# Kernel tuning notes

Measured on AMD Instinct MI355X. Metric: run time of the kernel, lower is better.

Reference implementation:

```python
import jax, jax.numpy as jnp
import numpy as np

B, S, E, H = 2, 2048, 1024, 16
D = E // H  # head_dim = 64


def setup_inputs() -> dict:
    key = jax.random.key(0)
    ks = jax.random.split(key, 14)
    inp = {
        "query": jax.random.normal(ks[0], (B, S, E), jnp.float32),
        "key": jax.random.normal(ks[1], (B, S, E), jnp.float32),
        "value": jax.random.normal(ks[2], (B, S, E), jnp.float32),
        "adj": jax.random.normal(ks[3], (S, S), jnp.float32),
        "mask": jax.random.randint(ks[4], (B, 1, S, S), 0, 2, jnp.int32),
    }
    sc = 1.0 / np.sqrt(E)
    inp["Wq"] = jax.random.normal(ks[5], (E, E), jnp.float32) * sc
    inp["bq"] = jax.random.normal(ks[6], (E,), jnp.float32) * sc
    inp["Wk"] = jax.random.normal(ks[7], (E, E), jnp.float32) * sc
    inp["bk"] = jax.random.normal(ks[8], (E,), jnp.float32) * sc
    inp["Wv"] = jax.random.normal(ks[9], (E, E), jnp.float32) * sc
    inp["bv"] = jax.random.normal(ks[10], (E,), jnp.float32) * sc
    inp["Wo"] = jax.random.normal(ks[11], (E, E), jnp.float32) * sc
    inp["bo"] = jax.random.normal(ks[12], (E,), jnp.float32) * sc
    return inp


def reference(query, key, value, adj, mask, Wq, bq, Wk, bk, Wv, bv, Wo, bo):
    b, s, _ = query.shape
    # projections, split into heads: [B,S,E] -> [B,H,S,D]
    def heads(x, W, bias):
        y = jnp.einsum("bse,ef->bsf", x, W.T) + bias
        return y.reshape(b, s, H, D).transpose(0, 2, 1, 3)

    Q = heads(query, Wq, bq)
    K = heads(key, Wk, bk)
    V = heads(value, Wv, bv)

    # scores: [B,H,S,S], scaled by sqrt(head_dim), plus adjacency bias
    scores = jnp.einsum("bhqd,bhkd->bhqk", Q, K) / jnp.sqrt(jnp.float32(D))
    scores = scores + adj[None, None, :, :]
    scores = jnp.where(mask == 0, jnp.float32(-jnp.inf), scores)

    weights = jax.nn.softmax(scores, axis=-1)
    out = jnp.einsum("bhqk,bhkd->bhqd", weights, V)
    out = out.transpose(0, 2, 1, 3).reshape(b, s, E)
    return jnp.einsum("bse,ef->bsf", out, Wo.T) + bo
```

## Files before the change

### kernel.cpp

```cpp
#include <hip/hip_runtime.h>


typedef unsigned short ushort_t;
typedef __attribute__((ext_vector_type(8))) short bf16x8;
typedef __attribute__((ext_vector_type(4))) float floatx4;
typedef __attribute__((ext_vector_type(2))) unsigned int uintx2;

#define NB 2
#define NS 2048
#define NE 1024
#define NH 16
#define ND 64
#define LOG2E 1.44269504f

__device__ __forceinline__ unsigned short f2bf(float f) {
  unsigned int u = __float_as_uint(f);
  return (unsigned short)((u + 0x7fffu + ((u >> 16) & 1u)) >> 16);
}
__device__ __forceinline__ float bf2f(unsigned short h) {
  return __uint_as_float(((unsigned int)h) << 16);
}

__device__ __forceinline__ void gload_lds16(const void* g, void* l) {
  __builtin_amdgcn_global_load_lds(
      (const __attribute__((address_space(1))) unsigned int*)g,
      (__attribute__((address_space(3))) unsigned int*)l, 16, 0, 0);
}

__device__ __forceinline__ uintx2 gload8(const void* p) {
  uintx2 r;
  asm volatile("global_load_dwordx2 %0, %1, off"
               : "=v"(r) : "v"(p) : "memory");
  return r;
}

__device__ __forceinline__ float fexp2(float x) {
#if __has_builtin(__builtin_amdgcn_exp2f)
  return __builtin_amdgcn_exp2f(x);
#else
  return exp2f(x);
#endif
}

__device__ __forceinline__ unsigned int cvtpk_bf16(float lo, float hi) {
  unsigned int r;
  asm("v_cvt_pk_bf16_f32 %0, %1, %2" : "=v"(r) : "v"(lo), "v"(hi));
  return r;
}

__device__ __forceinline__ void pl32swap(unsigned int& a, unsigned int& b) {
#if __has_builtin(__builtin_amdgcn_permlane32_swap)
  uintx2 r = __builtin_amdgcn_permlane32_swap(a, b, false, false);
  a = r[0]; b = r[1];
#else
  asm("v_permlane32_swap_b32 %0, %1" : "+v"(a), "+v"(b));
#endif
}
__device__ __forceinline__ void pl16swap(unsigned int& a, unsigned int& b) {
#if __has_builtin(__builtin_amdgcn_permlane16_swap)
  uintx2 r = __builtin_amdgcn_permlane16_swap(a, b, false, false);
  a = r[0]; b = r[1];
#else
  asm("v_permlane16_swap_b32 %0, %1" : "+v"(a), "+v"(b));
#endif
}

__global__ __launch_bounds__(256) void convert_kernel(
    const float* __restrict__ q, const float* __restrict__ k, const float* __restrict__ v,
    const float* __restrict__ wq, const float* __restrict__ wk,
    const float* __restrict__ wv, const float* __restrict__ wo,
    const float* __restrict__ adj, const int* __restrict__ mask,
    ushort_t* __restrict__ qb, ushort_t* __restrict__ kb, ushort_t* __restrict__ vb,
    ushort_t* __restrict__ wqb, ushort_t* __restrict__ wkb,
    ushort_t* __restrict__ wvb, ushort_t* __restrict__ wob,
    ushort_t* __restrict__ bias)
{
  const long U1 = (long)NB * NS * NE / 8;
  const long U2 = (long)NE * NE / 8;
  long idx = (long)blockIdx.x * 256 + threadIdx.x;
  const float* src;
  ushort_t* dst;
  if (idx < U1) { src = q; dst = qb; }
  else if ((idx -= U1) < U1) { src = k; dst = kb; }
  else if ((idx -= U1) < U1) { src = v; dst = vb; }
  else if ((idx -= U1) < U2) { src = wq; dst = wqb; }
  else if ((idx -= U2) < U2) { src = wk; dst = wkb; }
  else if ((idx -= U2) < U2) { src = wv; dst = wvb; }
  else if ((idx -= U2) < U2) { src = wo; dst = wob; }
  else {
    idx -= U2;
    long flat = idx * 8;
    long rem = flat & ((1L << 22) - 1);
    const float4* a4 = (const float4*)(adj + rem);
    const int4* m4 = (const int4*)(mask + flat);
    float4 a0 = a4[0], a1 = a4[1];
    int4 m0 = m4[0], m1 = m4[1];
    const float NEGV = -1e30f;
    union { ushort_t us[8]; uint4 v4; } o;
    o.us[0] = f2bf((m0.x ? a0.x : NEGV) * LOG2E);
    o.us[1] = f2bf((m0.y ? a0.y : NEGV) * LOG2E);
    o.us[2] = f2bf((m0.z ? a0.z : NEGV) * LOG2E);
    o.us[3] = f2bf((m0.w ? a0.w : NEGV) * LOG2E);
    o.us[4] = f2bf((m1.x ? a1.x : NEGV) * LOG2E);
    o.us[5] = f2bf((m1.y ? a1.y : NEGV) * LOG2E);
    o.us[6] = f2bf((m1.z ? a1.z : NEGV) * LOG2E);
    o.us[7] = f2bf((m1.w ? a1.w : NEGV) * LOG2E);
    ((uint4*)bias)[idx] = o.v4;
    return;
  }
  const float4* s4 = (const float4*)src;
  float4 a0 = s4[idx * 2], a1 = s4[idx * 2 + 1];
  union { ushort_t us[8]; uint4 v4; } o;
  o.us[0] = f2bf(a0.x); o.us[1] = f2bf(a0.y); o.us[2] = f2bf(a0.z); o.us[3] = f2bf(a0.w);
  o.us[4] = f2bf(a1.x); o.us[5] = f2bf(a1.y); o.us[6] = f2bf(a1.z); o.us[7] = f2bf(a1.w);
  ((uint4*)dst)[idx] = o.v4;
}

__global__ __launch_bounds__(256) void qkv_kernel(
    const ushort_t* __restrict__ xq, const ushort_t* __restrict__ xk, const ushort_t* __restrict__ xv,
    const ushort_t* __restrict__ wqb, const ushort_t* __restrict__ wkb, const ushort_t* __restrict__ wvb,
    const float* __restrict__ bq, const float* __restrict__ bk, const float* __restrict__ bvv,
    ushort_t* __restrict__ Qh, ushort_t* __restrict__ Kh, ushort_t* __restrict__ Vt)
{
  __shared__ __align__(16) ushort_t As[3][128 * 32];
  __shared__ __align__(16) ushort_t Bs[3][128 * 32];

  int z = blockIdx.z;
  const ushort_t* X = (z == 0) ? xq : (z == 1) ? xk : xv;
  const ushort_t* W = (z == 0) ? wqb : (z == 1) ? wkb : wvb;
  const float* bias = (z == 0) ? bq : (z == 1) ? bk : bvv;

  int t = threadIdx.x;
  int lane = t & 63, w = t >> 6;
  int quad = lane >> 4, l16 = lane & 15;
  int wr = w >> 1, wc = w & 1;
  int m0 = blockIdx.y * 128, f0 = blockIdx.x * 128;

  int arow = t >> 2, apart = t & 3;
  const ushort_t* Xg = X + (long)(m0 + arow) * NE + apart * 8;
  const ushort_t* Wg = W + (long)(f0 + arow) * NE + apart * 8;

  auto STAGE = [&](int kk, int buf) {
    int k0 = kk * 32;
    gload_lds16(Xg + k0, &As[buf][t * 8]);
    gload_lds16(Xg + k0 + 64 * NE, &As[buf][64 * 32 + t * 8]);
    gload_lds16(Wg + k0, &Bs[buf][t * 8]);
    gload_lds16(Wg + k0 + 64 * NE, &Bs[buf][64 * 32 + t * 8]);
  };
  STAGE(0, 0);
  STAGE(1, 1);

  floatx4 acc[4][4] = {};
  int b = 0;
  for (int k = 0; k < 32; ++k) {
    asm volatile("s_waitcnt vmcnt(4) lgkmcnt(0)" ::: "memory");
    __builtin_amdgcn_s_barrier();
    __builtin_amdgcn_sched_barrier(0);
    int nb = (b == 0) ? 2 : b - 1;
    STAGE((k + 2) & 31, nb);
    const ushort_t* Ab = As[b];
    const ushort_t* Bb = Bs[b];
    bf16x8 af[4], bf[4];
#pragma unroll
    for (int i = 0; i < 4; i++)
      af[i] = *(const bf16x8*)(Ab + (wr * 64 + i * 16 + l16) * 32 + quad * 8);
#pragma unroll
    for (int j = 0; j < 4; j++)
      bf[j] = *(const bf16x8*)(Bb + (wc * 64 + j * 16 + l16) * 32 + quad * 8);
#pragma unroll
    for (int i = 0; i < 4; i++)
#pragma unroll
      for (int j = 0; j < 4; j++)
        acc[i][j] = __builtin_amdgcn_mfma_f32_16x16x32_bf16(af[i], bf[j], acc[i][j], 0, 0, 0);
    b = (b == 2) ? 0 : b + 1;
  }
  asm volatile("s_waitcnt vmcnt(0)" ::: "memory");

  ushort_t* Out = (z == 0) ? Qh : (z == 1) ? Kh : Vt;
  bool isV = (z == 2);
#pragma unroll
  for (int j = 0; j < 4; j++) {
    int f = f0 + wc * 64 + j * 16 + l16;
    float bval = bias[f];
    int h = f >> 6, d = f & 63;
#pragma unroll
    for (int i = 0; i < 4; i++) {
      int mbase = m0 + wr * 64 + i * 16 + quad * 4;
#pragma unroll
      for (int r = 0; r < 4; r++) {
        int m = mbase + r;
        int bb2 = m >> 11, s = m & 2047;
        float y = acc[i][j][r] + bval;
        long off;
        if (!isV) off = ((long)(bb2 * NH + h) * NS + s) * ND + d;
        else      off = ((long)(bb2 * NH + h) * ND + d) * NS + s;
        Out[off] = f2bf(y);
      }
    }
  }
}

__global__ __launch_bounds__(256, 3) void attn_kernel(
    const ushort_t* __restrict__ Qh, const ushort_t* __restrict__ Kh,
    const ushort_t* __restrict__ Vt, const ushort_t* __restrict__ bias,
    ushort_t* __restrict__ PO, float* __restrict__ L)
{
  __shared__ __align__(16) ushort_t KVs[4][4096];

  int t = threadIdx.x, lane = t & 63, w = t >> 6;
  int quad = lane >> 4, l16 = lane & 15;
  int orig = blockIdx.x;
  int wg = ((orig & 7) << 7) | (orig >> 3);
  int h = wg & 15, g = wg >> 4;
  int ks = g & 1, qt = (g >> 1) & 15, bsel = g >> 5;
  int bh = bsel * NH + h;
  int q0 = qt * 128;
  int kbase = ks * (NS / 2);

  const ushort_t* Qg = Qh + ((long)bh * NS + q0) * ND;
  const ushort_t* Kg = Kh + ((long)bh * NS + kbase) * ND;
  const ushort_t* Vg = Vt + (long)bh * ND * NS + kbase;
  const ushort_t* biasg = bias + (long)bsel * NS * NS;

  bf16x8 aq[2][2];
#pragma unroll
  for (int m = 0; m < 2; m++)
#pragma unroll
    for (int kd = 0; kd < 2; kd++)
      aq[m][kd] = *(const bf16x8*)(Qg + (long)(w * 32 + m * 16 + l16) * ND
                                      + kd * 32 + quad * 8);

  int krow = t >> 3, kc = (t & 7) ^ (krow & 7);
  int vsr = t >> 3, vc2 = (t & 7) ^ (vsr & 7);
  int vrow = vsr * 2 + (vc2 >> 2), vpart = vc2 & 3;
  const ushort_t* Kgp = Kg + (long)krow * ND + kc * 8;
  const ushort_t* Vgp = Vg + (long)vrow * NS + vpart * 8;
  const ushort_t* pB0 = biasg + (long)(q0 + w * 32 + l16) * NS + kbase + quad * 4;
  const ushort_t* pB1 = pB0 + 16 * NS;

  auto STAGE = [&](int tile, int buf) {
    int k0 = tile * 32;
    gload_lds16(Kgp + (long)k0 * ND, &KVs[buf][t * 8]);
    gload_lds16(Vgp + k0, &KVs[buf][2048 + t * 8]);
  };
  uintx2 bcA[2][2], bcB[2][2];
  auto BLOAD = [&](uintx2 (&dst)[2][2], int tile) {
    long off = (long)tile * 32;
    dst[0][0] = gload8(pB0 + off);
    dst[0][1] = gload8(pB0 + off + 16);
    dst[1][0] = gload8(pB1 + off);
    dst[1][1] = gload8(pB1 + off + 16);
  };

  floatx4 acc[2][4] = {};
  float lsum[2] = {0.f, 0.f};
  const int ks_x = l16 & 7;
  const int vs_c = (((l16 & 1) * 4 + quad) ^ (l16 >> 1)) * 8;

  auto BODY = [&](const ushort_t* Kb, const ushort_t* Vb,
                  const uintx2 (&bcv)[2][2]) {
    bf16x8 bk[2][2], bv[4];
#pragma unroll
    for (int jk = 0; jk < 2; jk++)
#pragma unroll
      for (int kd = 0; kd < 2; kd++)
        bk[jk][kd] = *(const bf16x8*)(Kb + (jk * 16 + l16) * 64
                                         + ((kd * 4 + quad) ^ ks_x) * 8);
#pragma unroll
    for (int j = 0; j < 4; j++)
      bv[j] = *(const bf16x8*)(Vb + (j * 8 + (l16 >> 1)) * 64 + vs_c);
#pragma unroll
    for (int m = 0; m < 2; m++) {
      floatx4 sc[2] = {};
#pragma unroll
      for (int jk = 0; jk < 2; jk++)
#pragma unroll
        for (int kd = 0; kd < 2; kd++)
          sc[jk] = __builtin_amdgcn_mfma_f32_16x16x32_bf16(bk[jk][kd], aq[m][kd], sc[jk], 0, 0, 0);
      float p[2][4];
#pragma unroll
      for (int jk = 0; jk < 2; jk++) {
        unsigned int d0 = bcv[m][jk][0], d1 = bcv[m][jk][1];
        float b0 = __uint_as_float(d0 << 16);
        float b1 = __uint_as_float(d0 & 0xffff0000u);
        float b2 = __uint_as_float(d1 << 16);
        float b3 = __uint_as_float(d1 & 0xffff0000u);
        p[jk][0] = fexp2(fmaf(sc[jk][0], 0.125f * LOG2E, b0));
        p[jk][1] = fexp2(fmaf(sc[jk][1], 0.125f * LOG2E, b1));
        p[jk][2] = fexp2(fmaf(sc[jk][2], 0.125f * LOG2E, b2));
        p[jk][3] = fexp2(fmaf(sc[jk][3], 0.125f * LOG2E, b3));
      }
      lsum[m] += ((p[0][0] + p[0][1]) + (p[0][2] + p[0][3]))
               + ((p[1][0] + p[1][1]) + (p[1][2] + p[1][3]));
      unsigned int A0 = cvtpk_bf16(p[0][0], p[0][1]);
      unsigned int A1 = cvtpk_bf16(p[0][2], p[0][3]);
      unsigned int B0 = cvtpk_bf16(p[1][0], p[1][1]);
      unsigned int B1 = cvtpk_bf16(p[1][2], p[1][3]);
      pl32swap(A0, B0); pl16swap(A0, B0);
      pl32swap(A1, B1); pl16swap(A1, B1);
      union { unsigned int u[4]; bf16x8 v8; } pf;
      pf.u[0] = A0; pf.u[1] = A1; pf.u[2] = B0; pf.u[3] = B1;
#pragma unroll
      for (int j = 0; j < 4; j++)
        acc[m][j] = __builtin_amdgcn_mfma_f32_16x16x32_bf16(pf.v8, bv[j], acc[m][j], 0, 0, 0);
    }
  };

#define SB() __builtin_amdgcn_sched_barrier(0)
#define WAIT2()                                                   \
  asm volatile("s_waitcnt vmcnt(2) lgkmcnt(0)" ::: "memory");     \
  __builtin_amdgcn_s_barrier();                                   \
  SB()

  SB();
  asm volatile("s_waitcnt vmcnt(0)" ::: "memory");
  SB();
  STAGE(0, 0); SB();
  BLOAD(bcA, 0); SB();
  STAGE(1, 1); SB();

#pragma unroll 1
  for (int ii = 0; ii < 7; ++ii) {
    int base = ii * 4;
    WAIT2(); BLOAD(bcB, base + 1); SB(); STAGE(base + 2, 2); SB();
    BODY(&KVs[0][0], &KVs[0][2048], bcA);
    WAIT2(); BLOAD(bcA, base + 2); SB(); STAGE(base + 3, 3); SB();
    BODY(&KVs[1][0], &KVs[1][2048], bcB);
    WAIT2(); BLOAD(bcB, base + 3); SB(); STAGE(base + 4, 0); SB();
    BODY(&KVs[2][0], &KVs[2][2048], bcA);
    WAIT2(); BLOAD(bcA, base + 4); SB(); STAGE(base + 5, 1); SB();
    BODY(&KVs[3][0], &KVs[3][2048], bcB);
  }
  WAIT2(); BLOAD(bcB, 29); SB(); STAGE(30, 2); SB();
  BODY(&KVs[0][0], &KVs[0][2048], bcA);
  WAIT2(); BLOAD(bcA, 30); SB(); STAGE(31, 3); SB();
  BODY(&KVs[1][0], &KVs[1][2048], bcB);
  WAIT2(); BLOAD(bcB, 31); SB();
  BODY(&KVs[2][0], &KVs[2][2048], bcA);
  asm volatile("s_waitcnt vmcnt(0) lgkmcnt(0)" ::: "memory");
  __builtin_amdgcn_s_barrier();
  SB();
  BODY(&KVs[3][0], &KVs[3][2048], bcB);

#undef WAIT2
#undef SB

#pragma unroll
  for (int m = 0; m < 2; m++) {
    float s = lsum[m];
    s += __shfl_xor(s, 16);
    s += __shfl_xor(s, 32);
    lsum[m] = s;
  }

  ushort_t* pog = PO + (long)ks * 4194304 + (long)bh * 131072 + qt * 8192;
  float* Lg = L + ks * 65536 + bh * 2048 + qt * 128;
#pragma unroll
  for (int m = 0; m < 2; m++) {
#pragma unroll
    for (int r = 0; r < 4; r++) {
      float inv = 1.0f / __shfl(lsum[m], quad * 4 + r);
      int row = w * 32 + m * 16 + quad * 4 + r;
#pragma unroll
      for (int j = 0; j < 4; j++)
        pog[row * 64 + j * 16 + l16] = f2bf(acc[m][j][r] * inv);
    }
    if (quad == 0) Lg[w * 32 + m * 16 + l16] = lsum[m];
  }
}

__global__ __launch_bounds__(256) void combine_kernel(
    const ushort_t* __restrict__ PO, const float* __restrict__ L,
    ushort_t* __restrict__ aout)
{
  int idx = blockIdx.x * 256 + threadIdx.x;
  long f = (long)idx * 8;
  int r = (int)(f >> 6);
  float l0 = L[r], l1 = L[65536 + r];
  float inv = 1.0f / (l0 + l1);
  float w0 = l0 * inv, w1 = l1 * inv;
  union { uint4 v4; ushort_t us[8]; } ua, ub, o;
  ua.v4 = ((const uint4*)PO)[idx];
  ub.v4 = ((const uint4*)(PO + 4194304))[idx];
#pragma unroll
  for (int j = 0; j < 8; j++)
    o.us[j] = f2bf(w0 * bf2f(ua.us[j]) + w1 * bf2f(ub.us[j]));
  int q = r & 127, qt = (r >> 7) & 15, bh = r >> 11;
  int b_ = bh >> 4, h = bh & 15, d0 = (int)(f & 63);
  long off = (long)(b_ * NS + qt * 128 + q) * NE + h * ND + d0;
  *(uint4*)(aout + off) = o.v4;
}

__global__ __launch_bounds__(256) void oproj_kernel(
    const ushort_t* __restrict__ A, const ushort_t* __restrict__ Wob,
    const float* __restrict__ bo, float* __restrict__ out)
{
  __shared__ __align__(16) ushort_t As[3][128 * 32];
  __shared__ __align__(16) ushort_t Bs[3][64 * 32];

  int t = threadIdx.x;
  int lane = t & 63, w = t >> 6;
  int quad = lane >> 4, l16 = lane & 15;
  int wr = w >> 1, wc = w & 1;
  int m0 = blockIdx.y * 128, f0 = blockIdx.x * 64;

  int arow = t >> 2, apart = t & 3;
  const ushort_t* Xg = A + (long)(m0 + arow) * NE + apart * 8;
  const ushort_t* Wg = Wob + (long)(f0 + arow) * NE + apart * 8;

  auto STAGE = [&](int kk, int buf) {
    int k0 = kk * 32;
    gload_lds16(Xg + k0, &As[buf][t * 8]);
    gload_lds16(Xg + k0 + 64 * NE, &As[buf][64 * 32 + t * 8]);
    gload_lds16(Wg + k0, &Bs[buf][t * 8]);
  };
  STAGE(0, 0);
  STAGE(1, 1);

  floatx4 acc[4][2] = {};
  int b = 0;
  for (int k = 0; k < 32; ++k) {
    asm volatile("s_waitcnt vmcnt(3) lgkmcnt(0)" ::: "memory");
    __builtin_amdgcn_s_barrier();
    __builtin_amdgcn_sched_barrier(0);
    int nb = (b == 0) ? 2 : b - 1;
    STAGE((k + 2) & 31, nb);
    const ushort_t* Ab = As[b];
    const ushort_t* Bb = Bs[b];
    bf16x8 af[4], bf[2];
#pragma unroll
    for (int i = 0; i < 4; i++)
      af[i] = *(const bf16x8*)(Ab + (wr * 64 + i * 16 + l16) * 32 + quad * 8);
#pragma unroll
    for (int j = 0; j < 2; j++)
      bf[j] = *(const bf16x8*)(Bb + (wc * 32 + j * 16 + l16) * 32 + quad * 8);
#pragma unroll
    for (int i = 0; i < 4; i++)
#pragma unroll
      for (int j = 0; j < 2; j++)
        acc[i][j] = __builtin_amdgcn_mfma_f32_16x16x32_bf16(af[i], bf[j], acc[i][j], 0, 0, 0);
    b = (b == 2) ? 0 : b + 1;
  }
  asm volatile("s_waitcnt vmcnt(0)" ::: "memory");

#pragma unroll
  for (int j = 0; j < 2; j++) {
    int f = f0 + wc * 32 + j * 16 + l16;
    float bval = bo[f];
#pragma unroll
    for (int i = 0; i < 4; i++) {
      int mbase = m0 + wr * 64 + i * 16 + quad * 4;
#pragma unroll
      for (int r = 0; r < 4; r++) {
        int m = mbase + r;
        out[(long)m * NE + f] = acc[i][j][r] + bval;
      }
    }
  }
}

extern "C" void kernel_launch(void* const* d_in, const int* in_sizes, int n_in,
                              void* d_out, int out_size, void* d_ws, size_t ws_size,
                              hipStream_t stream) {
  const float* query = (const float*)d_in[0];
  const float* key   = (const float*)d_in[1];
  const float* value = (const float*)d_in[2];
  const float* adj   = (const float*)d_in[3];
  const int*   mask  = (const int*)d_in[4];
  const float* Wq = (const float*)d_in[5];
  const float* bq = (const float*)d_in[6];
  const float* Wk = (const float*)d_in[7];
  const float* bk = (const float*)d_in[8];
  const float* Wv = (const float*)d_in[9];
  const float* bv = (const float*)d_in[10];
  const float* Wo = (const float*)d_in[11];
  const float* bo = (const float*)d_in[12];
  float* out = (float*)d_out;

  char* ws = (char*)d_ws;
  const size_t MB = 1ull << 20;
  ushort_t* qb   = (ushort_t*)(ws + 0 * MB);
  ushort_t* kb   = (ushort_t*)(ws + 8 * MB);
  ushort_t* vb   = (ushort_t*)(ws + 16 * MB);
  ushort_t* wqb  = (ushort_t*)(ws + 24 * MB);
  ushort_t* wkb  = (ushort_t*)(ws + 26 * MB);
  ushort_t* wvb  = (ushort_t*)(ws + 28 * MB);
  ushort_t* wob  = (ushort_t*)(ws + 30 * MB);
  ushort_t* Qh   = (ushort_t*)(ws + 32 * MB);
  ushort_t* Kh   = (ushort_t*)(ws + 40 * MB);
  ushort_t* Vt   = (ushort_t*)(ws + 48 * MB);
  ushort_t* aout = (ushort_t*)(ws + 56 * MB);
  ushort_t* bias = (ushort_t*)(ws + 64 * MB);
  ushort_t* PO   = (ushort_t*)(ws + 0 * MB);
  float*    Lp   = (float*)(ws + 16 * MB);

  convert_kernel<<<12288, 256, 0, stream>>>(query, key, value, Wq, Wk, Wv, Wo,
                                            adj, mask, qb, kb, vb, wqb, wkb, wvb, wob, bias);
  qkv_kernel<<<dim3(8, 32, 3), 256, 0, stream>>>(qb, kb, vb, wqb, wkb, wvb,
                                                 bq, bk, bv, Qh, Kh, Vt);
  attn_kernel<<<dim3(1024), 256, 0, stream>>>(Qh, Kh, Vt, bias, PO, Lp);
  combine_kernel<<<dim3(2048), 256, 0, stream>>>(PO, Lp, aout);
  oproj_kernel<<<dim3(16, 32), 256, 0, stream>>>(aout, wob, bo, out);
}
```

Baseline: 316.4 us.

## Halve attention query tile to 64 rows and double workgroup count

```diff
diff --git a/kernel.cpp b/kernel.cpp
--- a/kernel.cpp
+++ b/kernel.cpp
@@ -210,11 +210,11 @@
   int t = threadIdx.x, lane = t & 63, w = t >> 6;
   int quad = lane >> 4, l16 = lane & 15;
   int orig = blockIdx.x;
-  int wg = ((orig & 7) << 7) | (orig >> 3);
+  int wg = ((orig & 7) << 8) | (orig >> 3);
   int h = wg & 15, g = wg >> 4;
-  int ks = g & 1, qt = (g >> 1) & 15, bsel = g >> 5;
+  int ks = g & 1, qt = (g >> 1) & 31, bsel = g >> 6;
   int bh = bsel * NH + h;
-  int q0 = qt * 128;
+  int q0 = qt * 64;
   int kbase = ks * (NS / 2);
 
   const ushort_t* Qg = Qh + ((long)bh * NS + q0) * ND;
@@ -222,43 +222,37 @@
   const ushort_t* Vg = Vt + (long)bh * ND * NS + kbase;
   const ushort_t* biasg = bias + (long)bsel * NS * NS;
 
-  bf16x8 aq[2][2];
-#pragma unroll
-  for (int m = 0; m < 2; m++)
-#pragma unroll
-    for (int kd = 0; kd < 2; kd++)
-      aq[m][kd] = *(const bf16x8*)(Qg + (long)(w * 32 + m * 16 + l16) * ND
-                                      + kd * 32 + quad * 8);
+  bf16x8 aq[2];
+#pragma unroll
+  for (int kd = 0; kd < 2; kd++)
+    aq[kd] = *(const bf16x8*)(Qg + (long)(w * 16 + l16) * ND + kd * 32 + quad * 8);
 
   int krow = t >> 3, kc = (t & 7) ^ (krow & 7);
   int vsr = t >> 3, vc2 = (t & 7) ^ (vsr & 7);
   int vrow = vsr * 2 + (vc2 >> 2), vpart = vc2 & 3;
   const ushort_t* Kgp = Kg + (long)krow * ND + kc * 8;
   const ushort_t* Vgp = Vg + (long)vrow * NS + vpart * 8;
-  const ushort_t* pB0 = biasg + (long)(q0 + w * 32 + l16) * NS + kbase + quad * 4;
-  const ushort_t* pB1 = pB0 + 16 * NS;
+  const ushort_t* pB0 = biasg + (long)(q0 + w * 16 + l16) * NS + kbase + quad * 4;
 
   auto STAGE = [&](int tile, int buf) {
     int k0 = tile * 32;
     gload_lds16(Kgp + (long)k0 * ND, &KVs[buf][t * 8]);
     gload_lds16(Vgp + k0, &KVs[buf][2048 + t * 8]);
   };
-  uintx2 bcA[2][2], bcB[2][2];
-  auto BLOAD = [&](uintx2 (&dst)[2][2], int tile) {
+  uintx2 bcA[2], bcB[2];
+  auto BLOAD = [&](uintx2 (&dst)[2], int tile) {
     long off = (long)tile * 32;
-    dst[0][0] = gload8(pB0 + off);
-    dst[0][1] = gload8(pB0 + off + 16);
-    dst[1][0] = gload8(pB1 + off);
-    dst[1][1] = gload8(pB1 + off + 16);
+    dst[0] = gload8(pB0 + off);
+    dst[1] = gload8(pB0 + off + 16);
   };
 
-  floatx4 acc[2][4] = {};
-  float lsum[2] = {0.f, 0.f};
+  floatx4 acc[4] = {};
+  float lsum = 0.f;
   const int ks_x = l16 & 7;
   const int vs_c = (((l16 & 1) * 4 + quad) ^ (l16 >> 1)) * 8;
 
   auto BODY = [&](const ushort_t* Kb, const ushort_t* Vb,
-                  const uintx2 (&bcv)[2][2]) {
+                  const uintx2 (&bcv)[2]) {
     bf16x8 bk[2][2], bv[4];
 #pragma unroll
     for (int jk = 0; jk < 2; jk++)
@@ -269,41 +263,39 @@
 #pragma unroll
     for (int j = 0; j < 4; j++)
       bv[j] = *(const bf16x8*)(Vb + (j * 8 + (l16 >> 1)) * 64 + vs_c);
-#pragma unroll
-    for (int m = 0; m < 2; m++) {
-      floatx4 sc[2] = {};
-#pragma unroll
-      for (int jk = 0; jk < 2; jk++)
-#pragma unroll
-        for (int kd = 0; kd < 2; kd++)
-          sc[jk] = __builtin_amdgcn_mfma_f32_16x16x32_bf16(bk[jk][kd], aq[m][kd], sc[jk], 0, 0, 0);
-      float p[2][4];
-#pragma unroll
-      for (int jk = 0; jk < 2; jk++) {
-        unsigned int d0 = bcv[m][jk][0], d1 = bcv[m][jk][1];
-        float b0 = __uint_as_float(d0 << 16);
-        float b1 = __uint_as_float(d0 & 0xffff0000u);
-        float b2 = __uint_as_float(d1 << 16);
-        float b3 = __uint_as_float(d1 & 0xffff0000u);
-        p[jk][0] = fexp2(fmaf(sc[jk][0], 0.125f * LOG2E, b0));
-        p[jk][1] = fexp2(fmaf(sc[jk][1], 0.125f * LOG2E, b1));
-        p[jk][2] = fexp2(fmaf(sc[jk][2], 0.125f * LOG2E, b2));
-        p[jk][3] = fexp2(fmaf(sc[jk][3], 0.125f * LOG2E, b3));
-      }
-      lsum[m] += ((p[0][0] + p[0][1]) + (p[0][2] + p[0][3]))
-               + ((p[1][0] + p[1][1]) + (p[1][2] + p[1][3]));
-      unsigned int A0 = cvtpk_bf16(p[0][0], p[0][1]);
-      unsigned int A1 = cvtpk_bf16(p[0][2], p[0][3]);
-      unsigned int B0 = cvtpk_bf16(p[1][0], p[1][1]);
-      unsigned int B1 = cvtpk_bf16(p[1][2], p[1][3]);
-      pl32swap(A0, B0); pl16swap(A0, B0);
-      pl32swap(A1, B1); pl16swap(A1, B1);
-      union { unsigned int u[4]; bf16x8 v8; } pf;
-      pf.u[0] = A0; pf.u[1] = A1; pf.u[2] = B0; pf.u[3] = B1;
-#pragma unroll
-      for (int j = 0; j < 4; j++)
-        acc[m][j] = __builtin_amdgcn_mfma_f32_16x16x32_bf16(pf.v8, bv[j], acc[m][j], 0, 0, 0);
+
+    floatx4 sc[2] = {};
+#pragma unroll
+    for (int jk = 0; jk < 2; jk++)
+#pragma unroll
+      for (int kd = 0; kd < 2; kd++)
+        sc[jk] = __builtin_amdgcn_mfma_f32_16x16x32_bf16(bk[jk][kd], aq[kd], sc[jk], 0, 0, 0);
+    float p[2][4];
+#pragma unroll
+    for (int jk = 0; jk < 2; jk++) {
+      unsigned int d0 = bcv[jk][0], d1 = bcv[jk][1];
+      float b0 = __uint_as_float(d0 << 16);
+      float b1 = __uint_as_float(d0 & 0xffff0000u);
+      float b2 = __uint_as_float(d1 << 16);
+      float b3 = __uint_as_float(d1 & 0xffff0000u);
+      p[jk][0] = fexp2(fmaf(sc[jk][0], 0.125f * LOG2E, b0));
+      p[jk][1] = fexp2(fmaf(sc[jk][1], 0.125f * LOG2E, b1));
+      p[jk][2] = fexp2(fmaf(sc[jk][2], 0.125f * LOG2E, b2));
+      p[jk][3] = fexp2(fmaf(sc[jk][3], 0.125f * LOG2E, b3));
     }
+    lsum += ((p[0][0] + p[0][1]) + (p[0][2] + p[0][3]))
+          + ((p[1][0] + p[1][1]) + (p[1][2] + p[1][3]));
+    unsigned int A0 = cvtpk_bf16(p[0][0], p[0][1]);
+    unsigned int A1 = cvtpk_bf16(p[0][2], p[0][3]);
+    unsigned int B0 = cvtpk_bf16(p[1][0], p[1][1]);
+    unsigned int B1 = cvtpk_bf16(p[1][2], p[1][3]);
+    pl32swap(A0, B0); pl16swap(A0, B0);
+    pl32swap(A1, B1); pl16swap(A1, B1);
+    union { unsigned int u[4]; bf16x8 v8; } pf;
+    pf.u[0] = A0; pf.u[1] = A1; pf.u[2] = B0; pf.u[3] = B1;
+#pragma unroll
+    for (int j = 0; j < 4; j++)
+      acc[j] = __builtin_amdgcn_mfma_f32_16x16x32_bf16(pf.v8, bv[j], acc[j], 0, 0, 0);
   };
 
 #define SB() __builtin_amdgcn_sched_barrier(0)
@@ -345,28 +337,24 @@
 #undef WAIT2
 #undef SB
 
-#pragma unroll
-  for (int m = 0; m < 2; m++) {
-    float s = lsum[m];
+  {
+    float s = lsum;
     s += __shfl_xor(s, 16);
     s += __shfl_xor(s, 32);
-    lsum[m] = s;
-  }
-
-  ushort_t* pog = PO + (long)ks * 4194304 + (long)bh * 131072 + qt * 8192;
-  float* Lg = L + ks * 65536 + bh * 2048 + qt * 128;
-#pragma unroll
-  for (int m = 0; m < 2; m++) {
-#pragma unroll
-    for (int r = 0; r < 4; r++) {
-      float inv = 1.0f / __shfl(lsum[m], quad * 4 + r);
-      int row = w * 32 + m * 16 + quad * 4 + r;
-#pragma unroll
-      for (int j = 0; j < 4; j++)
-        pog[row * 64 + j * 16 + l16] = f2bf(acc[m][j][r] * inv);
-    }
-    if (quad == 0) Lg[w * 32 + m * 16 + l16] = lsum[m];
-  }
+    lsum = s;
+  }
+
+  ushort_t* pog = PO + (long)ks * 4194304 + (long)bh * 131072 + qt * 4096;
+  float* Lg = L + ks * 65536 + bh * 2048 + qt * 64;
+#pragma unroll
+  for (int r = 0; r < 4; r++) {
+    float inv = 1.0f / __shfl(lsum, quad * 4 + r);
+    int row = w * 16 + quad * 4 + r;
+#pragma unroll
+    for (int j = 0; j < 4; j++)
+      pog[row * 64 + j * 16 + l16] = f2bf(acc[j][r] * inv);
+  }
+  if (quad == 0) Lg[w * 16 + l16] = lsum;
 }
 
 __global__ __launch_bounds__(256) void combine_kernel(
@@ -385,9 +373,9 @@
 #pragma unroll
   for (int j = 0; j < 8; j++)
     o.us[j] = f2bf(w0 * bf2f(ua.us[j]) + w1 * bf2f(ub.us[j]));
-  int q = r & 127, qt = (r >> 7) & 15, bh = r >> 11;
+  int q = r & 2047, bh = r >> 11;
   int b_ = bh >> 4, h = bh & 15, d0 = (int)(f & 63);
-  long off = (long)(b_ * NS + qt * 128 + q) * NE + h * ND + d0;
+  long off = (long)(b_ * NS + q) * NE + h * ND + d0;
   *(uint4*)(aout + off) = o.v4;
 }
 
@@ -498,7 +486,7 @@
                                             adj, mask, qb, kb, vb, wqb, wkb, wvb, wob, bias);
   qkv_kernel<<<dim3(8, 32, 3), 256, 0, stream>>>(qb, kb, vb, wqb, wkb, wvb,
                                                  bq, bk, bv, Qh, Kh, Vt);
-  attn_kernel<<<dim3(1024), 256, 0, stream>>>(Qh, Kh, Vt, bias, PO, Lp);
+  attn_kernel<<<dim3(2048), 256, 0, stream>>>(Qh, Kh, Vt, bias, PO, Lp);
   combine_kernel<<<dim3(2048), 256, 0, stream>>>(PO, Lp, aout);
   oproj_kernel<<<dim3(16, 32), 256, 0, stream>>>(aout, wob, bo, out);
 }
```

Result: slower. 322.8 us (+2.0%).

## Tile-reorder bias tensor and stage it through LDS with async loads

Applied to the files above, without the earlier changes.

```diff
diff --git a/kernel.cpp b/kernel.cpp
--- a/kernel.cpp
+++ b/kernel.cpp
@@ -25,13 +25,6 @@
   __builtin_amdgcn_global_load_lds(
       (const __attribute__((address_space(1))) unsigned int*)g,
       (__attribute__((address_space(3))) unsigned int*)l, 16, 0, 0);
-}
-
-__device__ __forceinline__ uintx2 gload8(const void* p) {
-  uintx2 r;
-  asm volatile("global_load_dwordx2 %0, %1, off"
-               : "=v"(r) : "v"(p) : "memory");
-  return r;
 }
 
 __device__ __forceinline__ float fexp2(float x) {
@@ -89,10 +82,15 @@
   else if ((idx -= U2) < U2) { src = wo; dst = wob; }
   else {
     idx -= U2;
-    long flat = idx * 8;
-    long rem = flat & ((1L << 22) - 1);
-    const float4* a4 = (const float4*)(adj + rem);
-    const int4* m4 = (const int4*)(mask + flat);
+    long u = idx;
+    int cp = (int)(u & 3);
+    int qq = (int)((u >> 2) & 2047);
+    int kt = (int)((u >> 13) & 63);
+    int b_ = (int)(u >> 19);
+    int lc = cp ^ ((qq >> 1) & 3);
+    int k0 = kt * 32 + lc * 8;
+    const float4* a4 = (const float4*)(adj + (long)qq * NS + k0);
+    const int4* m4 = (const int4*)(mask + (long)b_ * NS * NS + (long)qq * NS + k0);
     float4 a0 = a4[0], a1 = a4[1];
     int4 m0 = m4[0], m1 = m4[1];
     const float NEGV = -1e30f;
@@ -105,7 +103,7 @@
     o.us[5] = f2bf((m1.y ? a1.y : NEGV) * LOG2E);
     o.us[6] = f2bf((m1.z ? a1.z : NEGV) * LOG2E);
     o.us[7] = f2bf((m1.w ? a1.w : NEGV) * LOG2E);
-    ((uint4*)bias)[idx] = o.v4;
+    ((uint4*)bias)[u] = o.v4;
     return;
   }
   const float4* s4 = (const float4*)src;
@@ -205,7 +203,7 @@
     const ushort_t* __restrict__ Vt, const ushort_t* __restrict__ bias,
     ushort_t* __restrict__ PO, float* __restrict__ L)
 {
-  __shared__ __align__(16) ushort_t KVs[4][4096];
+  __shared__ __align__(16) ushort_t KVs[3][8192];
 
   int t = threadIdx.x, lane = t & 63, w = t >> 6;
   int quad = lane >> 4, l16 = lane & 15;
@@ -220,7 +218,7 @@
   const ushort_t* Qg = Qh + ((long)bh * NS + q0) * ND;
   const ushort_t* Kg = Kh + ((long)bh * NS + kbase) * ND;
   const ushort_t* Vg = Vt + (long)bh * ND * NS + kbase;
-  const ushort_t* biasg = bias + (long)bsel * NS * NS;
+  const ushort_t* Bg = bias + (((long)(bsel * 64 + ks * 32) * NS + q0) * 32);
 
   bf16x8 aq[2][2];
 #pragma unroll
@@ -235,21 +233,15 @@
   int vrow = vsr * 2 + (vc2 >> 2), vpart = vc2 & 3;
   const ushort_t* Kgp = Kg + (long)krow * ND + kc * 8;
   const ushort_t* Vgp = Vg + (long)vrow * NS + vpart * 8;
-  const ushort_t* pB0 = biasg + (long)(q0 + w * 32 + l16) * NS + kbase + quad * 4;
-  const ushort_t* pB1 = pB0 + 16 * NS;
+  const ushort_t* Bgp = Bg + t * 8;
 
   auto STAGE = [&](int tile, int buf) {
     int k0 = tile * 32;
     gload_lds16(Kgp + (long)k0 * ND, &KVs[buf][t * 8]);
     gload_lds16(Vgp + k0, &KVs[buf][2048 + t * 8]);
-  };
-  uintx2 bcA[2][2], bcB[2][2];
-  auto BLOAD = [&](uintx2 (&dst)[2][2], int tile) {
-    long off = (long)tile * 32;
-    dst[0][0] = gload8(pB0 + off);
-    dst[0][1] = gload8(pB0 + off + 16);
-    dst[1][0] = gload8(pB1 + off);
-    dst[1][1] = gload8(pB1 + off + 16);
+    const ushort_t* bsrc = Bgp + (long)tile * 65536;
+    gload_lds16(bsrc, &KVs[buf][4096 + t * 8]);
+    gload_lds16(bsrc + 2048, &KVs[buf][4096 + 2048 + t * 8]);
   };
 
   floatx4 acc[2][4] = {};
@@ -257,8 +249,10 @@
   const int ks_x = l16 & 7;
   const int vs_c = (((l16 & 1) * 4 + quad) ^ (l16 >> 1)) * 8;
 
-  auto BODY = [&](const ushort_t* Kb, const ushort_t* Vb,
-                  const uintx2 (&bcv)[2][2]) {
+  auto BODY = [&](int buf) {
+    const ushort_t* Kb = &KVs[buf][0];
+    const ushort_t* Vb = &KVs[buf][2048];
+    const ushort_t* Bb = &KVs[buf][4096];
     bf16x8 bk[2][2], bv[4];
 #pragma unroll
     for (int jk = 0; jk < 2; jk++)
@@ -277,14 +271,20 @@
 #pragma unroll
         for (int kd = 0; kd < 2; kd++)
           sc[jk] = __builtin_amdgcn_mfma_f32_16x16x32_bf16(bk[jk][kd], aq[m][kd], sc[jk], 0, 0, 0);
+      int qq = w * 32 + m * 16 + l16;
+      int px = (qq >> 1) & 3;
+      int hb = (quad & 1) * 4;
+      uintx2 d0v = *(const uintx2*)(Bb + qq * 32 + (((quad >> 1) ^ px) * 8) + hb);
+      uintx2 d1v = *(const uintx2*)(Bb + qq * 32 + (((2 + (quad >> 1)) ^ px) * 8) + hb);
       float p[2][4];
 #pragma unroll
       for (int jk = 0; jk < 2; jk++) {
-        unsigned int d0 = bcv[m][jk][0], d1 = bcv[m][jk][1];
-        float b0 = __uint_as_float(d0 << 16);
-        float b1 = __uint_as_float(d0 & 0xffff0000u);
-        float b2 = __uint_as_float(d1 << 16);
-        float b3 = __uint_as_float(d1 & 0xffff0000u);
+        unsigned int e0 = (jk == 0) ? d0v[0] : d1v[0];
+        unsigned int e1 = (jk == 0) ? d0v[1] : d1v[1];
+        float b0 = __uint_as_float(e0 << 16);
+        float b1 = __uint_as_float(e0 & 0xffff0000u);
+        float b2 = __uint_as_float(e1 << 16);
+        float b3 = __uint_as_float(e1 & 0xffff0000u);
         p[jk][0] = fexp2(fmaf(sc[jk][0], 0.125f * LOG2E, b0));
         p[jk][1] = fexp2(fmaf(sc[jk][1], 0.125f * LOG2E, b1));
         p[jk][2] = fexp2(fmaf(sc[jk][2], 0.125f * LOG2E, b2));
@@ -307,8 +307,8 @@
   };
 
 #define SB() __builtin_amdgcn_sched_barrier(0)
-#define WAIT2()                                                   \
-  asm volatile("s_waitcnt vmcnt(2) lgkmcnt(0)" ::: "memory");     \
+#define WAIT4()                                                   \
+  asm volatile("s_waitcnt vmcnt(4) lgkmcnt(0)" ::: "memory");     \
   __builtin_amdgcn_s_barrier();                                   \
   SB()
 
@@ -316,33 +316,22 @@
   asm volatile("s_waitcnt vmcnt(0)" ::: "memory");
   SB();
   STAGE(0, 0); SB();
-  BLOAD(bcA, 0); SB();
   STAGE(1, 1); SB();
 
 #pragma unroll 1
-  for (int ii = 0; ii < 7; ++ii) {
-    int base = ii * 4;
-    WAIT2(); BLOAD(bcB, base + 1); SB(); STAGE(base + 2, 2); SB();
-    BODY(&KVs[0][0], &KVs[0][2048], bcA);
-    WAIT2(); BLOAD(bcA, base + 2); SB(); STAGE(base + 3, 3); SB();
-    BODY(&KVs[1][0], &KVs[1][2048], bcB);
-    WAIT2(); BLOAD(bcB, base + 3); SB(); STAGE(base + 4, 0); SB();
-    BODY(&KVs[2][0], &KVs[2][2048], bcA);
-    WAIT2(); BLOAD(bcA, base + 4); SB(); STAGE(base + 5, 1); SB();
-    BODY(&KVs[3][0], &KVs[3][2048], bcB);
-  }
-  WAIT2(); BLOAD(bcB, 29); SB(); STAGE(30, 2); SB();
-  BODY(&KVs[0][0], &KVs[0][2048], bcA);
-  WAIT2(); BLOAD(bcA, 30); SB(); STAGE(31, 3); SB();
-  BODY(&KVs[1][0], &KVs[1][2048], bcB);
-  WAIT2(); BLOAD(bcB, 31); SB();
-  BODY(&KVs[2][0], &KVs[2][2048], bcA);
+  for (int ii = 0; ii < 10; ++ii) {
+    int base = ii * 3;
+    WAIT4(); STAGE(base + 2, 2); SB(); BODY(0);
+    WAIT4(); STAGE(base + 3, 0); SB(); BODY(1);
+    WAIT4(); STAGE(base + 4, 1); SB(); BODY(2);
+  }
+  WAIT4(); BODY(0);
   asm volatile("s_waitcnt vmcnt(0) lgkmcnt(0)" ::: "memory");
   __builtin_amdgcn_s_barrier();
   SB();
-  BODY(&KVs[3][0], &KVs[3][2048], bcB);
-
-#undef WAIT2
+  BODY(1);
+
+#undef WAIT4
 #undef SB
 
 #pragma unroll
```

Result: faster. 292.8 us (-7.4%).
